# Performance work log

Hardware: AMD Instinct MI355X
Metric: run time of the kernel (lower is better)

The kernel has to match this reference:

```python
import jax, jax.numpy as jnp
import numpy as np

WINDOW_SIZES = [1, 3]
PROXIMITY = 8
VOCAB = 30522


def setup_inputs() -> dict:
    key = jax.random.key(0)
    k0, k1, k2, k3, k4, k5 = jax.random.split(key, 6)
    B, Q, D, P = 16, 32, 256, 8
    q_tok_ids = jax.random.randint(k0, (B, Q), 0, VOCAB, dtype=jnp.int32)
    q_tok_weights = jax.random.uniform(k1, (B, Q), dtype=jnp.float32)
    d_tok_ids = jax.random.randint(k2, (B, D), 0, VOCAB, dtype=jnp.int32)
    d_logits = jax.random.normal(k3, (B, D, VOCAB), dtype=jnp.float32)
    # CSR-style passage-group offsets: P=8 groups of 2 passages each
    psg_offset = (jnp.arange(P + 1, dtype=jnp.int32) * (B // P))
    lin_w = jax.random.normal(k4, (1, 2 * len(WINDOW_SIZES) - 1), dtype=jnp.float32)
    lin_b = jax.random.normal(k5, (1,), dtype=jnp.float32)
    return {"q_tok_ids": q_tok_ids, "q_tok_weights": q_tok_weights,
            "d_tok_ids": d_tok_ids, "d_logits": d_logits,
            "psg_offset": psg_offset, "lin_w": lin_w, "lin_b": lin_b}


def _score_pairs(q_tok_ids, q_tok_weights, d_tok_ids, d_logits, psg_offset, lin_w, lin_b):
    B, Q = q_tok_ids.shape
    # gather document logits at query token ids: d_logits[b, d, q_ids[b, q]]
    g = jnp.take_along_axis(d_logits, q_tok_ids[:, None, :].astype(jnp.int32), axis=2)  # [B, D, Q]
    trans = q_tok_weights[:, :, None] * jnp.swapaxes(g, 1, 2)  # [B, Q, D]
    # the torch scatter-mask keeps d_logits[b,d,v] only where v == d_tok_ids[b,d];
    # gathering the masked logits at q_tok_ids is equivalent to an id-equality mask
    exact = trans * (q_tok_ids[:, :, None] == d_tok_ids[:, None, :]).astype(trans.dtype)
    all_scores = [trans.max(axis=2).sum(axis=1)]
    # ordered n-gram windows (diagonal shifts on both q and d axes)
    for wsize in WINDOW_SIZES[1:]:
        sm = exact
        mk = (exact > 0).astype(trans.dtype)
        for i in range(1, wsize):
            sm = sm[:, :-1, :-1] + exact[:, i:, i:]
            mk = mk[:, :-1, :-1] * (exact[:, i:, i:] > 0)
        all_scores.append((sm * mk).max(axis=2).sum(axis=1))
    # unordered proximity: sliding max over the document axis
    prox = exact
    for i in range(1, PROXIMITY):
        prox = jnp.maximum(prox[:, :, :-1], exact[:, :, i:])
    for wsize in WINDOW_SIZES[1:]:
        sm = prox
        mk = (prox > 0).astype(trans.dtype)
        for i in range(1, wsize):
            sm = sm[:, :-1, :] + prox[:, i:, :]
            mk = mk[:, :-1, :] * (prox[:, i:, :] > 0)
        all_scores.append((sm * mk).max(axis=2).sum(axis=1))
    all_scores = jnp.stack(all_scores, axis=1)  # [B, 2*len(ws)-1]
    # ragged segment-max over passage groups defined by psg_offset
    P = psg_offset.shape[0] - 1
    seg_ids = jnp.sum(jnp.arange(B)[:, None] >= psg_offset[None, 1:-1], axis=1)
    max_psg = jax.ops.segment_max(all_scores, seg_ids, num_segments=P)  # [P, F]
    return max_psg @ lin_w[0] + lin_b[0]  # [P]


def reference(q_tok_ids, q_tok_weights, d_tok_ids, d_logits, psg_offset, lin_w, lin_b):
    return _score_pairs(q_tok_ids, q_tok_weights, d_tok_ids, d_logits, psg_offset, lin_w, lin_b)
```

## Files before the change

### kernel.cpp

```cpp
#include <hip/hip_runtime.h>
#include <float.h>

#define B_  16
#define Q_  32
#define D_  256
#define V_  30522
#define F_  3
#define PROX 8

__global__ __launch_bounds__(256) void score_kernel(
    const int*   __restrict__ qids,
    const float* __restrict__ qw,
    const int*   __restrict__ dids,
    const float* __restrict__ dlog,
    float*       __restrict__ scores)
{
    __shared__ int   s_qid[Q_];
    __shared__ float s_qw[Q_];
    __shared__ int   s_did[D_];
    __shared__ float s_tr[Q_][D_ + 1];
    __shared__ float s_part[4][F_];

    const int b    = blockIdx.x;
    const int tid  = threadIdx.x;
    const int lane = tid & 63;
    const int wave = tid >> 6;

    if (tid < Q_) { s_qid[tid] = qids[b * Q_ + tid]; s_qw[tid] = qw[b * Q_ + tid]; }
    s_did[tid] = dids[b * D_ + tid];
    __syncthreads();

    {
        const float* base = dlog + (size_t)b * D_ * V_ + (size_t)tid * V_;
        #pragma unroll
        for (int q = 0; q < Q_; ++q) {
            s_tr[q][tid] = base[s_qid[q]] * s_qw[q];
        }
    }
    __syncthreads();

    float sum0 = 0.f;
    #pragma unroll
    for (int r = 0; r < 8; ++r) {
        const int q = wave * 8 + r;
        float m = -FLT_MAX;
        for (int d = lane; d < D_; d += 64) m = fmaxf(m, s_tr[q][d]);
        #pragma unroll
        for (int off = 32; off; off >>= 1) m = fmaxf(m, __shfl_xor(m, off));
        sum0 += m;
    }

    float sum1 = 0.f;
    for (int q = wave; q < Q_ - 2; q += 4) {
        const int qa = s_qid[q], qb = s_qid[q + 1], qc = s_qid[q + 2];
        float m = 0.f;
        for (int d = lane; d < D_ - 2; d += 64) {
            const float e0 = (qa == s_did[d])     ? s_tr[q][d]         : 0.f;
            const float e1 = (qb == s_did[d + 1]) ? s_tr[q + 1][d + 1] : 0.f;
            const float e2 = (qc == s_did[d + 2]) ? s_tr[q + 2][d + 2] : 0.f;
            const float v  = (e0 > 0.f && e1 > 0.f && e2 > 0.f) ? (e0 + e1 + e2) : 0.f;
            m = fmaxf(m, v);
        }
        #pragma unroll
        for (int off = 32; off; off >>= 1) m = fmaxf(m, __shfl_xor(m, off));
        sum1 += m;
    }

    float px[Q_];
    const int d0 = tid;
    if (d0 < D_ - PROX + 1) {
        #pragma unroll
        for (int q = 0; q < Q_; ++q) {
            const int qid = s_qid[q];
            float m = -FLT_MAX;
            #pragma unroll
            for (int i = 0; i < PROX; ++i) {
                const float e = (qid == s_did[d0 + i]) ? s_tr[q][d0 + i] : 0.f;
                m = fmaxf(m, e);
            }
            px[q] = m;
        }
    }
    __syncthreads();
    if (d0 < D_ - PROX + 1) {
        #pragma unroll
        for (int q = 0; q < Q_; ++q) s_tr[q][d0] = px[q];
    }
    __syncthreads();

    float sum2 = 0.f;
    for (int q = wave; q < Q_ - 2; q += 4) {
        float m = 0.f;
        for (int d = lane; d < D_ - PROX + 1; d += 64) {
            const float p0 = s_tr[q][d], p1 = s_tr[q + 1][d], p2 = s_tr[q + 2][d];
            const float v  = (p0 > 0.f && p1 > 0.f && p2 > 0.f) ? (p0 + p1 + p2) : 0.f;
            m = fmaxf(m, v);
        }
        #pragma unroll
        for (int off = 32; off; off >>= 1) m = fmaxf(m, __shfl_xor(m, off));
        sum2 += m;
    }

    if (lane == 0) { s_part[wave][0] = sum0; s_part[wave][1] = sum1; s_part[wave][2] = sum2; }
    __syncthreads();
    if (tid == 0) {
        float a0 = 0.f, a1 = 0.f, a2 = 0.f;
        #pragma unroll
        for (int w = 0; w < 4; ++w) { a0 += s_part[w][0]; a1 += s_part[w][1]; a2 += s_part[w][2]; }
        scores[b * F_ + 0] = a0;
        scores[b * F_ + 1] = a1;
        scores[b * F_ + 2] = a2;
    }
}

__global__ void finalize_kernel(
    const float* __restrict__ scores,
    const int*   __restrict__ poff,
    const float* __restrict__ lw,
    const float* __restrict__ lb,
    float*       __restrict__ out,
    int P)
{
    const int p = threadIdx.x;
    if (p < P) {
        const int lo = poff[p], hi = poff[p + 1];
        float m0 = -FLT_MAX, m1 = -FLT_MAX, m2 = -FLT_MAX;
        for (int b = lo; b < hi; ++b) {
            m0 = fmaxf(m0, scores[b * F_ + 0]);
            m1 = fmaxf(m1, scores[b * F_ + 1]);
            m2 = fmaxf(m2, scores[b * F_ + 2]);
        }
        out[p] = m0 * lw[0] + m1 * lw[1] + m2 * lw[2] + lb[0];
    }
}

extern "C" void kernel_launch(void* const* d_in, const int* in_sizes, int n_in,
                              void* d_out, int out_size, void* d_ws, size_t ws_size,
                              hipStream_t stream) {
    const int*   qids = (const int*)  d_in[0];
    const float* qw   = (const float*)d_in[1];
    const int*   dids = (const int*)  d_in[2];
    const float* dlog = (const float*)d_in[3];
    const int*   poff = (const int*)  d_in[4];
    const float* lw   = (const float*)d_in[5];
    const float* lb   = (const float*)d_in[6];
    float* out    = (float*)d_out;
    float* scores = (float*)d_ws;

    score_kernel<<<B_, 256, 0, stream>>>(qids, qw, dids, dlog, scores);
    const int P = in_sizes[4] - 1;
    finalize_kernel<<<1, 64, 0, stream>>>(scores, poff, lw, lb, out, P);
}
```

Baseline: 35.04 us.

## Split random gather into wide kernel and fuse finalize via last-block atomic

The scattered gather of document logits at query ids moves into its own kernel launched with 256 blocks instead of 16, so many more loads are in flight across the GPU. Its results go to a workspace buffer, which the score kernel reads back with coalesced float4 loads into shared memory. The separate finalize kernel is folded into the score kernel using an atomic counter, so the last block to finish computes the segment max and linear layer. This trades one extra launch plus a workspace round trip for much higher memory-level parallelism on the latency-bound gather. It also drops the shared-memory row padding, which may add bank conflicts on later accesses.

Measured after the change: 35.20 us, median of 3. About the same (+0.4%).

```diff
diff --git a/kernel.cpp b/kernel.cpp
--- a/kernel.cpp
+++ b/kernel.cpp
@@ -8,34 +8,65 @@
 #define F_  3
 #define PROX 8
 
+__global__ __launch_bounds__(256) void gather_kernel(
+    const int*   __restrict__ qids,
+    const float* __restrict__ qw,
+    const float* __restrict__ dlog,
+    float*       __restrict__ tr,
+    int*         __restrict__ counter)
+{
+    if (blockIdx.x == 0 && threadIdx.x == 0) *counter = 0;
+
+    const int b   = blockIdx.x >> 4;
+    const int c0  = (blockIdx.x & 15) << 4;
+    const int tid = threadIdx.x;
+    const int d   = c0 + (tid & 15);
+    const int q0  = tid >> 4;
+
+    __shared__ int   s_qid[Q_];
+    __shared__ float s_qw[Q_];
+    if (tid < Q_) { s_qid[tid] = qids[b * Q_ + tid]; s_qw[tid] = qw[b * Q_ + tid]; }
+    __syncthreads();
+
+    const float* base = dlog + (size_t)b * D_ * V_ + (size_t)d * V_;
+    const float v0 = base[s_qid[q0]]      * s_qw[q0];
+    const float v1 = base[s_qid[q0 + 16]] * s_qw[q0 + 16];
+    tr[(b * Q_ + q0     ) * D_ + d] = v0;
+    tr[(b * Q_ + q0 + 16) * D_ + d] = v1;
+}
+
 __global__ __launch_bounds__(256) void score_kernel(
     const int*   __restrict__ qids,
-    const float* __restrict__ qw,
     const int*   __restrict__ dids,
-    const float* __restrict__ dlog,
-    float*       __restrict__ scores)
+    const float* __restrict__ tr,
+    const int*   __restrict__ poff,
+    const float* __restrict__ lw,
+    const float* __restrict__ lb,
+    float*       __restrict__ scores,
+    int*         __restrict__ counter,
+    float*       __restrict__ out,
+    int P)
 {
     __shared__ int   s_qid[Q_];
-    __shared__ float s_qw[Q_];
     __shared__ int   s_did[D_];
-    __shared__ float s_tr[Q_][D_ + 1];
+    __shared__ float s_tr[Q_][D_];
     __shared__ float s_part[4][F_];
+    __shared__ int   s_last;
 
     const int b    = blockIdx.x;
     const int tid  = threadIdx.x;
     const int lane = tid & 63;
     const int wave = tid >> 6;
 
-    if (tid < Q_) { s_qid[tid] = qids[b * Q_ + tid]; s_qw[tid] = qw[b * Q_ + tid]; }
+    if (tid < Q_) s_qid[tid] = qids[b * Q_ + tid];
     s_did[tid] = dids[b * D_ + tid];
-    __syncthreads();
 
     {
-        const float* base = dlog + (size_t)b * D_ * V_ + (size_t)tid * V_;
+        float* s_flat = &s_tr[0][0];
+        const float* trb = tr + (size_t)b * Q_ * D_;
         #pragma unroll
-        for (int q = 0; q < Q_; ++q) {
-            s_tr[q][tid] = base[s_qid[q]] * s_qw[q];
-        }
+        for (int i = tid * 4; i < Q_ * D_; i += 256 * 4)
+            *(float4*)&s_flat[i] = *(const float4*)&trb[i];
     }
     __syncthreads();
 
@@ -110,27 +141,24 @@
         scores[b * F_ + 0] = a0;
         scores[b * F_ + 1] = a1;
         scores[b * F_ + 2] = a2;
+        __threadfence();
+        const int prev = atomicAdd(counter, 1);
+        s_last = (prev == B_ - 1) ? 1 : 0;
     }
-}
+    __syncthreads();
 
-__global__ void finalize_kernel(
-    const float* __restrict__ scores,
-    const int*   __restrict__ poff,
-    const float* __restrict__ lw,
-    const float* __restrict__ lb,
-    float*       __restrict__ out,
-    int P)
-{
-    const int p = threadIdx.x;
-    if (p < P) {
-        const int lo = poff[p], hi = poff[p + 1];
-        float m0 = -FLT_MAX, m1 = -FLT_MAX, m2 = -FLT_MAX;
-        for (int b = lo; b < hi; ++b) {
-            m0 = fmaxf(m0, scores[b * F_ + 0]);
-            m1 = fmaxf(m1, scores[b * F_ + 1]);
-            m2 = fmaxf(m2, scores[b * F_ + 2]);
+    if (s_last) {
+        __threadfence();
+        if (tid < P) {
+            const int lo = poff[tid], hi = poff[tid + 1];
+            float m0 = -FLT_MAX, m1 = -FLT_MAX, m2 = -FLT_MAX;
+            for (int bb = lo; bb < hi; ++bb) {
+                m0 = fmaxf(m0, scores[bb * F_ + 0]);
+                m1 = fmaxf(m1, scores[bb * F_ + 1]);
+                m2 = fmaxf(m2, scores[bb * F_ + 2]);
+            }
+            out[tid] = m0 * lw[0] + m1 * lw[1] + m2 * lw[2] + lb[0];
         }
-        out[p] = m0 * lw[0] + m1 * lw[1] + m2 * lw[2] + lb[0];
     }
 }
 
@@ -144,10 +172,14 @@
     const int*   poff = (const int*)  d_in[4];
     const float* lw   = (const float*)d_in[5];
     const float* lb   = (const float*)d_in[6];
-    float* out    = (float*)d_out;
-    float* scores = (float*)d_ws;
+    float* out = (float*)d_out;
 
-    score_kernel<<<B_, 256, 0, stream>>>(qids, qw, dids, dlog, scores);
+    float* tr      = (float*)d_ws;
+    float* scores  = (float*)((char*)d_ws + B_ * Q_ * D_ * 4);
+    int*   counter = (int*)  ((char*)d_ws + B_ * Q_ * D_ * 4 + B_ * F_ * 4);
+
+    gather_kernel<<<B_ * 16, 256, 0, stream>>>(qids, qw, dlog, tr, counter);
     const int P = in_sizes[4] - 1;
-    finalize_kernel<<<1, 64, 0, stream>>>(scores, poff, lw, lb, out, P);
+    score_kernel<<<B_, 256, 0, stream>>>(qids, dids, tr, poff, lw, lb,
+                                         scores, counter, out, P);
 }
```

## Fuse scoring and segment-max finalize into one kernel per passage group

Applied to the files above, without the earlier changes.

Replaces the per-batch scoring kernel plus the separate finalize kernel with a single kernel launched per passage group. Each block loops serially over its batch rows and keeps a running per-feature max in shared memory before applying the linear layer. This removes one kernel launch and the workspace round trip. In exchange it halves the grid and serializes the latency-bound logit gathers within each block. The shared-memory row padding is also dropped.

Result: slower. 59.58 us (+70.0%).

```diff
diff --git a/kernel.cpp b/kernel.cpp
--- a/kernel.cpp
+++ b/kernel.cpp
@@ -8,130 +8,122 @@
 #define F_  3
 #define PROX 8
 
-__global__ __launch_bounds__(256) void score_kernel(
+__global__ __launch_bounds__(256) void fused_kernel(
     const int*   __restrict__ qids,
     const float* __restrict__ qw,
     const int*   __restrict__ dids,
     const float* __restrict__ dlog,
-    float*       __restrict__ scores)
+    const int*   __restrict__ poff,
+    const float* __restrict__ lw,
+    const float* __restrict__ lb,
+    float*       __restrict__ out)
 {
     __shared__ int   s_qid[Q_];
     __shared__ float s_qw[Q_];
     __shared__ int   s_did[D_];
-    __shared__ float s_tr[Q_][D_ + 1];
+    __shared__ float s_tr[Q_][D_];
     __shared__ float s_part[4][F_];
+    __shared__ float s_best[F_];
 
-    const int b    = blockIdx.x;
+    const int p    = blockIdx.x;
+    const int lo   = poff[p], hi = poff[p + 1];
     const int tid  = threadIdx.x;
     const int lane = tid & 63;
     const int wave = tid >> 6;
 
-    if (tid < Q_) { s_qid[tid] = qids[b * Q_ + tid]; s_qw[tid] = qw[b * Q_ + tid]; }
-    s_did[tid] = dids[b * D_ + tid];
-    __syncthreads();
+    if (tid == 0) { s_best[0] = -FLT_MAX; s_best[1] = -FLT_MAX; s_best[2] = -FLT_MAX; }
 
-    {
-        const float* base = dlog + (size_t)b * D_ * V_ + (size_t)tid * V_;
+    for (int b = lo; b < hi; ++b) {
+        __syncthreads();
+        if (tid < Q_) { s_qid[tid] = qids[b * Q_ + tid]; s_qw[tid] = qw[b * Q_ + tid]; }
+        s_did[tid] = dids[b * D_ + tid];
+        __syncthreads();
+
+        {
+            const float* base = dlog + (size_t)b * D_ * V_ + (size_t)tid * V_;
+            #pragma unroll
+            for (int q = 0; q < Q_; ++q)
+                s_tr[q][tid] = base[s_qid[q]] * s_qw[q];
+        }
+        __syncthreads();
+
+        float sum0 = 0.f;
         #pragma unroll
-        for (int q = 0; q < Q_; ++q) {
-            s_tr[q][tid] = base[s_qid[q]] * s_qw[q];
+        for (int r = 0; r < 8; ++r) {
+            const int q = wave * 8 + r;
+            float m = -FLT_MAX;
+            for (int d = lane; d < D_; d += 64) m = fmaxf(m, s_tr[q][d]);
+            #pragma unroll
+            for (int off = 32; off; off >>= 1) m = fmaxf(m, __shfl_xor(m, off));
+            sum0 += m;
+        }
+
+        float sum1 = 0.f;
+        for (int q = wave; q < Q_ - 2; q += 4) {
+            const int qa = s_qid[q], qb = s_qid[q + 1], qc = s_qid[q + 2];
+            float m = 0.f;
+            for (int d = lane; d < D_ - 2; d += 64) {
+                const float e0 = (qa == s_did[d])     ? s_tr[q][d]         : 0.f;
+                const float e1 = (qb == s_did[d + 1]) ? s_tr[q + 1][d + 1] : 0.f;
+                const float e2 = (qc == s_did[d + 2]) ? s_tr[q + 2][d + 2] : 0.f;
+                const float v  = (e0 > 0.f && e1 > 0.f && e2 > 0.f) ? (e0 + e1 + e2) : 0.f;
+                m = fmaxf(m, v);
+            }
+            #pragma unroll
+            for (int off = 32; off; off >>= 1) m = fmaxf(m, __shfl_xor(m, off));
+            sum1 += m;
+        }
+
+        float px[Q_];
+        const int d0 = tid;
+        if (d0 < D_ - PROX + 1) {
+            #pragma unroll
+            for (int q = 0; q < Q_; ++q) {
+                const int qid = s_qid[q];
+                float m = -FLT_MAX;
+                #pragma unroll
+                for (int i = 0; i < PROX; ++i) {
+                    const float e = (qid == s_did[d0 + i]) ? s_tr[q][d0 + i] : 0.f;
+                    m = fmaxf(m, e);
+                }
+                px[q] = m;
+            }
+        }
+        __syncthreads();
+        if (d0 < D_ - PROX + 1) {
+            #pragma unroll
+            for (int q = 0; q < Q_; ++q) s_tr[q][d0] = px[q];
+        }
+        __syncthreads();
+
+        float sum2 = 0.f;
+        for (int q = wave; q < Q_ - 2; q += 4) {
+            float m = 0.f;
+            for (int d = lane; d < D_ - PROX + 1; d += 64) {
+                const float p0 = s_tr[q][d], p1 = s_tr[q + 1][d], p2 = s_tr[q + 2][d];
+                const float v  = (p0 > 0.f && p1 > 0.f && p2 > 0.f) ? (p0 + p1 + p2) : 0.f;
+                m = fmaxf(m, v);
+            }
+            #pragma unroll
+            for (int off = 32; off; off >>= 1) m = fmaxf(m, __shfl_xor(m, off));
+            sum2 += m;
+        }
+
+        if (lane == 0) { s_part[wave][0] = sum0; s_part[wave][1] = sum1; s_part[wave][2] = sum2; }
+        __syncthreads();
+        if (tid == 0) {
+            float a0 = 0.f, a1 = 0.f, a2 = 0.f;
+            #pragma unroll
+            for (int w = 0; w < 4; ++w) { a0 += s_part[w][0]; a1 += s_part[w][1]; a2 += s_part[w][2]; }
+            s_best[0] = fmaxf(s_best[0], a0);
+            s_best[1] = fmaxf(s_best[1], a1);
+            s_best[2] = fmaxf(s_best[2], a2);
         }
     }
+
     __syncthreads();
-
-    float sum0 = 0.f;
-    #pragma unroll
-    for (int r = 0; r < 8; ++r) {
-        const int q = wave * 8 + r;
-        float m = -FLT_MAX;
-        for (int d = lane; d < D_; d += 64) m = fmaxf(m, s_tr[q][d]);
-        #pragma unroll
-        for (int off = 32; off; off >>= 1) m = fmaxf(m, __shfl_xor(m, off));
-        sum0 += m;
-    }
-
-    float sum1 = 0.f;
-    for (int q = wave; q < Q_ - 2; q += 4) {
-        const int qa = s_qid[q], qb = s_qid[q + 1], qc = s_qid[q + 2];
-        float m = 0.f;
-        for (int d = lane; d < D_ - 2; d += 64) {
-            const float e0 = (qa == s_did[d])     ? s_tr[q][d]         : 0.f;
-            const float e1 = (qb == s_did[d + 1]) ? s_tr[q + 1][d + 1] : 0.f;
-            const float e2 = (qc == s_did[d + 2]) ? s_tr[q + 2][d + 2] : 0.f;
-            const float v  = (e0 > 0.f && e1 > 0.f && e2 > 0.f) ? (e0 + e1 + e2) : 0.f;
-            m = fmaxf(m, v);
-        }
-        #pragma unroll
-        for (int off = 32; off; off >>= 1) m = fmaxf(m, __shfl_xor(m, off));
-        sum1 += m;
-    }
-
-    float px[Q_];
-    const int d0 = tid;
-    if (d0 < D_ - PROX + 1) {
-        #pragma unroll
-        for (int q = 0; q < Q_; ++q) {
-            const int qid = s_qid[q];
-            float m = -FLT_MAX;
-            #pragma unroll
-            for (int i = 0; i < PROX; ++i) {
-                const float e = (qid == s_did[d0 + i]) ? s_tr[q][d0 + i] : 0.f;
-                m = fmaxf(m, e);
-            }
-            px[q] = m;
-        }
-    }
-    __syncthreads();
-    if (d0 < D_ - PROX + 1) {
-        #pragma unroll
-        for (int q = 0; q < Q_; ++q) s_tr[q][d0] = px[q];
-    }
-    __syncthreads();
-
-    float sum2 = 0.f;
-    for (int q = wave; q < Q_ - 2; q += 4) {
-        float m = 0.f;
-        for (int d = lane; d < D_ - PROX + 1; d += 64) {
-            const float p0 = s_tr[q][d], p1 = s_tr[q + 1][d], p2 = s_tr[q + 2][d];
-            const float v  = (p0 > 0.f && p1 > 0.f && p2 > 0.f) ? (p0 + p1 + p2) : 0.f;
-            m = fmaxf(m, v);
-        }
-        #pragma unroll
-        for (int off = 32; off; off >>= 1) m = fmaxf(m, __shfl_xor(m, off));
-        sum2 += m;
-    }
-
-    if (lane == 0) { s_part[wave][0] = sum0; s_part[wave][1] = sum1; s_part[wave][2] = sum2; }
-    __syncthreads();
-    if (tid == 0) {
-        float a0 = 0.f, a1 = 0.f, a2 = 0.f;
-        #pragma unroll
-        for (int w = 0; w < 4; ++w) { a0 += s_part[w][0]; a1 += s_part[w][1]; a2 += s_part[w][2]; }
-        scores[b * F_ + 0] = a0;
-        scores[b * F_ + 1] = a1;
-        scores[b * F_ + 2] = a2;
-    }
-}
-
-__global__ void finalize_kernel(
-    const float* __restrict__ scores,
-    const int*   __restrict__ poff,
-    const float* __restrict__ lw,
-    const float* __restrict__ lb,
-    float*       __restrict__ out,
-    int P)
-{
-    const int p = threadIdx.x;
-    if (p < P) {
-        const int lo = poff[p], hi = poff[p + 1];
-        float m0 = -FLT_MAX, m1 = -FLT_MAX, m2 = -FLT_MAX;
-        for (int b = lo; b < hi; ++b) {
-            m0 = fmaxf(m0, scores[b * F_ + 0]);
-            m1 = fmaxf(m1, scores[b * F_ + 1]);
-            m2 = fmaxf(m2, scores[b * F_ + 2]);
-        }
-        out[p] = m0 * lw[0] + m1 * lw[1] + m2 * lw[2] + lb[0];
-    }
+    if (tid == 0)
+        out[p] = s_best[0] * lw[0] + s_best[1] * lw[1] + s_best[2] * lw[2] + lb[0];
 }
 
 extern "C" void kernel_launch(void* const* d_in, const int* in_sizes, int n_in,
@@ -144,10 +136,8 @@
     const int*   poff = (const int*)  d_in[4];
     const float* lw   = (const float*)d_in[5];
     const float* lb   = (const float*)d_in[6];
-    float* out    = (float*)d_out;
-    float* scores = (float*)d_ws;
+    float* out = (float*)d_out;
 
-    score_kernel<<<B_, 256, 0, stream>>>(qids, qw, dids, dlog, scores);
     const int P = in_sizes[4] - 1;
-    finalize_kernel<<<1, 64, 0, stream>>>(scores, poff, lw, lb, out, P);
+    fused_kernel<<<P, 256, 0, stream>>>(qids, qw, dids, dlog, poff, lw, lb, out);
 }
```
